# Performance work log

Hardware: AMD Instinct MI355X
Metric: run time of the kernel (lower is better)

Reference implementation:

```python
import jax, jax.numpy as jnp
import numpy as np

EMBED_DIMS = [8, 16, 8]      # prod = 1024 = embed_dim
HIDDEN_DIMS = [16, 16, 16]   # prod = 4096 = hidden_dim
RANK = 16
B, S = 4, 1024


def _make_cores(key, in_dims, out_dims, rank):
    d = len(in_dims)
    ranks = [1] + [rank] * (d - 1) + [1]
    cores = []
    for k in range(d):
        key, sub = jax.random.split(key)
        shape = (ranks[k], in_dims[k], out_dims[k], ranks[k + 1])
        scale = 1.0 / np.sqrt(in_dims[k] * ranks[k])
        cores.append((scale * jax.random.normal(sub, shape, dtype=jnp.float32)))
    return cores


def setup_inputs() -> dict:
    key = jax.random.key(0)
    k_x, k1, k2, kb1, kb2 = jax.random.split(key, 5)
    x = jax.random.normal(k_x, (B, S, 1024), dtype=jnp.float32)
    fc1 = _make_cores(k1, EMBED_DIMS, HIDDEN_DIMS, RANK)
    fc2 = _make_cores(k2, HIDDEN_DIMS, EMBED_DIMS, RANK)
    b1 = 0.01 * jax.random.normal(kb1, (4096,), dtype=jnp.float32)
    b2 = 0.01 * jax.random.normal(kb2, (1024,), dtype=jnp.float32)
    return {
        "x": x,
        "fc1_c0": fc1[0], "fc1_c1": fc1[1], "fc1_c2": fc1[2], "fc1_b": b1,
        "fc2_c0": fc2[0], "fc2_c1": fc2[1], "fc2_c2": fc2[2], "fc2_b": b2,
    }


def tt_linear(x_flat, cores, bias, in_dims):
    """TT-matrix x batch-of-vectors product. x_flat: [N, prod(in_dims)].

    Cores: core_k has shape [r_{k-1}, n_k, m_k, r_k] with r_0 = r_d = 1.
    Invariant: acc is [r_{k-1}, n_k, rest] with rest laid out as
    (n_{k+1}..n_d, N, m_1..m_{k-1}).
    """
    N = x_flat.shape[0]
    acc = x_flat.reshape((N,) + tuple(in_dims))      # [N, n1..nd]
    acc = jnp.moveaxis(acc, 0, -1)                   # [n1..nd, N]
    acc = acc.reshape(in_dims[0], -1)[None]          # [1, n1, rest]
    d = len(cores)
    for k, c in enumerate(cores):
        # contract previous rank + current input mode
        acc = jnp.einsum('pnR,pnmq->Rmq', acc, c)    # [rest, m_k, r_k]
        if k < d - 1:
            n_next = in_dims[k + 1]
            R, m, q = acc.shape
            acc = acc.reshape(n_next, R // n_next, m, q)
            acc = jnp.transpose(acc, (3, 0, 1, 2)).reshape(q, n_next, -1)
    # final acc: [N * m1..m_{d-1}, m_d, 1] -> [N, M]
    return acc.reshape(N, -1) + bias


def reference(x, fc1_c0, fc1_c1, fc1_c2, fc1_b, fc2_c0, fc2_c1, fc2_c2, fc2_b):
    flat = x.reshape(-1, x.shape[-1])                        # [N, embed_dim]
    z1 = tt_linear(flat, [fc1_c0, fc1_c1, fc1_c2], fc1_b, EMBED_DIMS)   # [N, hidden]
    h1 = jax.nn.gelu(z1, approximate=False)                  # exact erf GELU (torch default)
    z2 = tt_linear(h1, [fc2_c0, fc2_c1, fc2_c2], fc2_b, HIDDEN_DIMS)    # [N, embed]
    return z2.reshape(*x.shape[:-1], z2.shape[-1])
```

## Files before the change

kernel.cpp:

```cpp
#include <hip/hip_runtime.h>
#include <stdint.h>

__device__ __forceinline__ float b2f(unsigned short u) {
    union { uint32_t i; float f; } v; v.i = ((uint32_t)u) << 16; return v.f;
}
__device__ __forceinline__ unsigned short f2b(float f) {
    union { float f; uint32_t i; } v; v.f = f;
    uint32_t r = v.i + 0x7fffu + ((v.i >> 16) & 1u);
    return (unsigned short)(r >> 16);
}

typedef __bf16 bf16x8 __attribute__((ext_vector_type(8)));
typedef float  f32x16 __attribute__((ext_vector_type(16)));

template<int N1, int N2, int N3, int M1, int M2, int M3>
__device__ __forceinline__ void build_W_fused(int blk,
                                              const float* __restrict__ c0,
                                              const float* __restrict__ c1,
                                              const float* __restrict__ c2,
                                              unsigned short* __restrict__ W,
                                              float* __restrict__ S) {
    constexpr int K = N1 * N2 * N3;
    const int n2 = blk / M2;
    const int m2 = blk % M2;

    for (int e = threadIdx.x; e < 16 * N3 * M3; e += 256) {
        const int m3 = e % M3;
        const int n3 = (e / M3) % N3;
        const int r1 = e / (M3 * N3);
        const float* c1p = c1 + ((r1 * N2 + n2) * M2 + m2) * 16;
        float s = 0.f;
#pragma unroll
        for (int r2 = 0; r2 < 16; ++r2)
            s += c1p[r2] * c2[(r2 * N3 + n3) * M3 + m3];
        S[e] = s;
    }
    __syncthreads();

    for (int e = threadIdx.x; e < N1 * M1 * M3; e += 256) {
        const int m3 = e % M3;
        const int m1 = (e / M3) % M1;
        const int n1 = e / (M3 * M1);
        const float* c0p = c0 + (n1 * M1 + m1) * 16;
        float acc[N3] = {};
#pragma unroll
        for (int r1 = 0; r1 < 16; ++r1) {
            const float c0v = c0p[r1];
#pragma unroll
            for (int n3 = 0; n3 < N3; ++n3)
                acc[n3] += c0v * S[(r1 * N3 + n3) * M3 + m3];
        }
        unsigned short ob[N3];
#pragma unroll
        for (int n3 = 0; n3 < N3; ++n3) ob[n3] = f2b(acc[n3]);
        unsigned short* dst = W + (size_t)((m1 * M2 + m2) * M3 + m3) * K
                                + (n1 * N2 + n2) * N3;
#pragma unroll
        for (int c = 0; c < N3 / 8; ++c)
            ((int4*)dst)[c] = ((const int4*)ob)[c];
    }
}

__global__ __launch_bounds__(256)
void prep_all(const float* __restrict__ c10, const float* __restrict__ c11,
              const float* __restrict__ c12,
              const float* __restrict__ c20, const float* __restrict__ c21,
              const float* __restrict__ c22,
              const float* __restrict__ x, unsigned short* __restrict__ xb,
              unsigned short* __restrict__ W1, unsigned short* __restrict__ W2) {
    __shared__ float S[16 * 128];
    const int b = blockIdx.x;
    if (b < 256) {
        build_W_fused<8, 16, 8, 16, 16, 16>(b, c10, c11, c12, W1, S);
    } else if (b < 512) {
        build_W_fused<16, 16, 16, 8, 16, 8>(b - 256, c20, c21, c22, W2, S);
    } else {
        const int t = (b - 512) * 256 + threadIdx.x;
        const float4* p = (const float4*)(x + (size_t)t * 8);
        float4 f0 = p[0], f1 = p[1];
        int4 o;
        o.x = (uint32_t)f2b(f0.x) | ((uint32_t)f2b(f0.y) << 16);
        o.y = (uint32_t)f2b(f0.z) | ((uint32_t)f2b(f0.w) << 16);
        o.z = (uint32_t)f2b(f1.x) | ((uint32_t)f2b(f1.y) << 16);
        o.w = (uint32_t)f2b(f1.z) | ((uint32_t)f2b(f1.w) << 16);
        ((int4*)xb)[t] = o;
    }
}

template<int N3, int M3>
__device__ __forceinline__ void build_T_body(int e,
                                             const float* __restrict__ c1,
                                             const float* __restrict__ c2,
                                             float* __restrict__ T) {
    int m3 = e % M3;
    int t  = e / M3;
    int n3 = t % N3;
    int rm = t / N3;
    float s = 0.f;
#pragma unroll
    for (int r2 = 0; r2 < 16; ++r2)
        s += c1[rm * 16 + r2] * c2[(r2 * N3 + n3) * M3 + m3];
    T[e] = s;
}

__global__ __launch_bounds__(256)
void prep_stage1(const float* __restrict__ c11, const float* __restrict__ c12,
                 float* __restrict__ T1,
                 const float* __restrict__ c21, const float* __restrict__ c22,
                 float* __restrict__ T2,
                 const float* __restrict__ x, unsigned short* __restrict__ xb) {
    const int b = blockIdx.x;
    if (b < 2048) {
        build_T_body<8, 16>(b * 256 + threadIdx.x, c11, c12, T1);
    } else if (b < 4096) {
        build_T_body<16, 8>((b - 2048) * 256 + threadIdx.x, c21, c22, T2);
    } else {
        const int t = (b - 4096) * 256 + threadIdx.x;
        const float4* p = (const float4*)(x + (size_t)t * 8);
        float4 f0 = p[0], f1 = p[1];
        int4 o;
        o.x = (uint32_t)f2b(f0.x) | ((uint32_t)f2b(f0.y) << 16);
        o.y = (uint32_t)f2b(f0.z) | ((uint32_t)f2b(f0.w) << 16);
        o.z = (uint32_t)f2b(f1.x) | ((uint32_t)f2b(f1.y) << 16);
        o.w = (uint32_t)f2b(f1.z) | ((uint32_t)f2b(f1.w) << 16);
        ((int4*)xb)[t] = o;
    }
}

template<int N1, int N2, int N3, int M1, int M2, int M3>
__device__ __forceinline__ void build_W_body(int t,
                                             const float* __restrict__ c0,
                                             const float* __restrict__ T,
                                             unsigned short* __restrict__ W) {
    constexpr int K = N1 * N2 * N3;
    int m3 = t % M3;
    int m2 = (t / M3) % M2;
    int n2 = (t / (M3 * M2)) % N2;
    int m1 = (t / (M3 * M2 * N2)) % M1;
    int n1 =  t / (M3 * M2 * N2 * M1);

    float c0r[16];
    const float4* c0p = (const float4*)(c0 + (n1 * M1 + m1) * 16);
#pragma unroll
    for (int i = 0; i < 4; ++i) ((float4*)c0r)[i] = c0p[i];

    float acc[N3] = {};
#pragma unroll
    for (int r1 = 0; r1 < 16; ++r1) {
        const float* Tp = T + (size_t)(((r1 * 16 + n2) * 16 + m2) * N3) * M3 + m3;
#pragma unroll
        for (int n3 = 0; n3 < N3; ++n3)
            acc[n3] += c0r[r1] * Tp[n3 * M3];
    }

    unsigned short ob[N3];
#pragma unroll
    for (int n3 = 0; n3 < N3; ++n3) ob[n3] = f2b(acc[n3]);

    unsigned short* dst = W + (size_t)((m1 * M2 + m2) * M3 + m3) * K
                            + (n1 * N2 + n2) * N3;
#pragma unroll
    for (int c = 0; c < N3 / 8; ++c)
        ((int4*)dst)[c] = ((const int4*)ob)[c];
}

template<int N1, int N2, int N3, int M1, int M2, int M3>
__global__ __launch_bounds__(256)
void build_W(const float* __restrict__ c0, const float* __restrict__ T,
             unsigned short* __restrict__ W) {
    build_W_body<N1, N2, N3, M1, M2, M3>(blockIdx.x * 256 + threadIdx.x, c0, T, W);
}

template<int BM, int BN, int KTOT, int GX, bool DO_GELU>
__global__ __launch_bounds__(512, 2)
void gemm_8p(const unsigned short* __restrict__ A,
             const unsigned short* __restrict__ Bt,
             const float* __restrict__ bias,
             unsigned short* __restrict__ C,
             int Ncols)
{
    constexpr int BK   = 64;
    constexpr int NT   = KTOT / BK;
    constexpr int AE   = BM * BK;
    constexpr int SLOT = (BM + BN) * BK;
    constexpr int ACH  = (AE * 2) / 1024;
    constexpr int CPW  = ((SLOT * 2) / 1024) / 8;

    extern __shared__ unsigned short sh[];

    const int tid   = threadIdx.x;
    const int lane  = tid & 63;
    const int wave  = tid >> 6;
    const int m32   = lane & 31;
    const int kh    = lane >> 5;
    const int waveM = (wave >> 1) * 64;
    const int waveN = (wave & 1) * 64;
    const int srow8 = lane >> 3;
    const int sslot = lane & 7;

    int lin = (int)blockIdx.y * GX + (int)blockIdx.x;
    const int total = GX * (int)gridDim.y;
    lin = (lin & 7) * (total >> 3) + (lin >> 3);
    const int colBase = (lin % GX) * BN;
    const int rowBase = (lin / GX) * BM;

#define P8_STAGE(TS_, KK_, U_)                                                \
    {                                                                         \
        const int c_   = wave * CPW + (U_);                                   \
        const bool b_  = c_ >= ACH;                                           \
        const int r_   = (b_ ? c_ - ACH : c_) * 8 + srow8;                    \
        const int jg_  = sslot ^ (r_ & 7) ^ ((r_ >> 3) & 7);                  \
        const unsigned short* s_ = (b_ ?                                      \
            Bt + (size_t)(colBase + r_) * KTOT :                              \
            A  + (size_t)(rowBase + r_) * KTOT) + (KK_) + jg_ * 8;            \
        unsigned short* d_ = sh + (TS_) + c_ * 512;                           \
        __builtin_amdgcn_global_load_lds(                                     \
            (const __attribute__((address_space(1))) void*)s_,                \
            (__attribute__((address_space(3))) void*)d_, 16, 0, 0);           \
    }

    f32x16 acc[2][2] = {};

#pragma unroll
    for (int u = 0; u < CPW; ++u) P8_STAGE(0, 0, u)
#pragma unroll
    for (int u = 0; u < CPW; ++u) P8_STAGE(SLOT, BK, u)
    asm volatile("s_waitcnt vmcnt(%0)" :: "n"(CPW) : "memory");
    __builtin_amdgcn_s_barrier();

    for (int t = 0; t < NT; ++t) {
        const unsigned short* Ab = sh + (t % 3) * SLOT;
        const unsigned short* Bb = Ab + AE;
        const int ts = ((t + 2) % 3) * SLOT;
        const int kk = (t + 2) * BK;
        const bool doStage = (t + 2 < NT);

#pragma unroll
        for (int ph = 0; ph < 4; ++ph) {
            bf16x8 af[2], bfr[2];
            const int g = ph * 2 + kh;
#pragma unroll
            for (int i = 0; i < 2; ++i) {
                const int r = waveM + i * 32 + m32;
                const int key = (r & 7) ^ ((r >> 3) & 7);
                af[i] = *(const bf16x8*)&Ab[r * BK + ((g ^ key) << 3)];
            }
#pragma unroll
            for (int j = 0; j < 2; ++j) {
                const int r = waveN + j * 32 + m32;
                const int key = (r & 7) ^ ((r >> 3) & 7);
                bfr[j] = *(const bf16x8*)&Bb[r * BK + ((g ^ key) << 3)];
            }
            if (doStage && ph < 3) {
                P8_STAGE(ts, kk, ph * 2)
                P8_STAGE(ts, kk, ph * 2 + 1)
            }
            __builtin_amdgcn_s_barrier();
            __builtin_amdgcn_s_setprio(1);
#pragma unroll
            for (int i = 0; i < 2; ++i)
#pragma unroll
                for (int j = 0; j < 2; ++j)
                    acc[i][j] = __builtin_amdgcn_mfma_f32_32x32x16_bf16(
                        af[i], bfr[j], acc[i][j], 0, 0, 0);
            __builtin_amdgcn_s_setprio(0);
            __builtin_amdgcn_s_barrier();
        }

        if (t + 2 < NT) {
            asm volatile("s_waitcnt vmcnt(%0)" :: "n"(CPW) : "memory");
        } else if (t + 1 < NT) {
            asm volatile("s_waitcnt vmcnt(0)" ::: "memory");
        }
        if (t + 1 < NT) __builtin_amdgcn_s_barrier();
    }
#undef P8_STAGE

#pragma unroll
    for (int i = 0; i < 2; ++i) {
#pragma unroll
        for (int j = 0; j < 2; ++j) {
            const int col = colBase + waveN + j * 32 + m32;
            const float bv = bias[col];
#pragma unroll
            for (int reg = 0; reg < 16; ++reg) {
                const int row = rowBase + waveM + i * 32 +
                                (reg & 3) + 8 * (reg >> 2) + 4 * kh;
                float z = acc[i][j][reg] + bv;
                if (DO_GELU)
                    z = 0.5f * z * (1.f + erff(z * 0.70710678118654752f));
                C[(size_t)row * Ncols + col] = f2b(z);
            }
        }
    }
}

template<int BM, int BN, int KCH, int KSTR, int GX, int GY,
         bool DO_GELU, bool ATOMIC>
__global__ __launch_bounds__(256, 4)
void gemm_sb(const unsigned short* __restrict__ A,
             const unsigned short* __restrict__ Bt,
             const float* __restrict__ bias,
             void* __restrict__ Cv,
             int Ncols)
{
    constexpr int BK  = 64;
    constexpr int NT  = KCH / BK;
    constexpr int ASZ = BM * BK;
    constexpr int ACH = BM / 32;
    constexpr int BCH = BN / 32;
    constexpr int FI  = BM / 64, FJ = BN / 64;

    extern __shared__ unsigned short sh[];

    const int tid   = threadIdx.x;
    const int lane  = tid & 63;
    const int wave  = tid >> 6;
    const int m32   = lane & 31;
    const int khalf = lane >> 5;
    const int waveM = (wave >> 1) * (BM / 2);
    const int waveN = (wave & 1) * (BN / 2);
    const int srow  = tid >> 3;
    const int sslot = tid & 7;

    int lin = ((int)blockIdx.z * GY + (int)blockIdx.y) * GX + (int)blockIdx.x;
    const int total = GX * GY * (int)gridDim.z;
    lin = (lin & 7) * (total >> 3) + (lin >> 3);
    const int colBase = (lin % GX) * BN;
    const int rowBase = ((lin / GX) % GY) * BM;
    const int kOff    = (lin / (GX * GY)) * KCH;

#define SB_STAGE(K0_)                                                         \
    {                                                                         \
        _Pragma("unroll")                                                     \
        for (int c = 0; c < ACH; ++c) {                                       \
            const int r  = c * 32 + srow;                                     \
            const int jg = sslot ^ (r & 7) ^ ((r >> 3) & 7);                  \
            const unsigned short* src = A +                                   \
                (size_t)(rowBase + r) * KSTR + (K0_) + jg * 8;                \
            unsigned short* dst = sh + c * 2048 + wave * 512;                 \
            __builtin_amdgcn_global_load_lds(                                 \
                (const __attribute__((address_space(1))) void*)src,           \
                (__attribute__((address_space(3))) void*)dst, 16, 0, 0);      \
        }                                                                     \
        _Pragma("unroll")                                                     \
        for (int c = 0; c < BCH; ++c) {                                       \
            const int r  = c * 32 + srow;                                     \
            const int jg = sslot ^ (r & 7) ^ ((r >> 3) & 7);                  \
            const unsigned short* src = Bt +                                  \
                (size_t)(colBase + r) * KSTR + (K0_) + jg * 8;                \
            unsigned short* dst = sh + ASZ + c * 2048 + wave * 512;           \
            __builtin_amdgcn_global_load_lds(                                 \
                (const __attribute__((address_space(1))) void*)src,           \
                (__attribute__((address_space(3))) void*)dst, 16, 0, 0);      \
        }                                                                     \
    }

    f32x16 acc[FI][FJ] = {};

    for (int t = 0; t < NT; ++t) {
        SB_STAGE(kOff + t * BK)
        __syncthreads();

        const unsigned short* Ab = sh;
        const unsigned short* Bb = sh + ASZ;
#pragma unroll
        for (int ks = 0; ks < 4; ++ks) {
            bf16x8 a_f[FI], b_f[FJ];
            const int g = ks * 2 + khalf;
#pragma unroll
            for (int i = 0; i < FI; ++i) {
                const int r = waveM + i * 32 + m32;
                const int key = (r & 7) ^ ((r >> 3) & 7);
                a_f[i] = *(const bf16x8*)&Ab[r * BK + ((g ^ key) << 3)];
            }
#pragma unroll
            for (int j = 0; j < FJ; ++j) {
                const int r = waveN + j * 32 + m32;
                const int key = (r & 7) ^ ((r >> 3) & 7);
                b_f[j] = *(const bf16x8*)&Bb[r * BK + ((g ^ key) << 3)];
            }
#pragma unroll
            for (int i = 0; i < FI; ++i)
#pragma unroll
                for (int j = 0; j < FJ; ++j)
                    acc[i][j] = __builtin_amdgcn_mfma_f32_32x32x16_bf16(
                        a_f[i], b_f[j], acc[i][j], 0, 0, 0);
        }
        if (t + 1 < NT) __syncthreads();
    }
#undef SB_STAGE

#pragma unroll
    for (int i = 0; i < FI; ++i) {
#pragma unroll
        for (int j = 0; j < FJ; ++j) {
            const int col = colBase + waveN + j * 32 + m32;
            const float bv = ATOMIC ? 0.f : bias[col];
#pragma unroll
            for (int reg = 0; reg < 16; ++reg) {
                const int row = rowBase + waveM + i * 32 +
                                (reg & 3) + 8 * (reg >> 2) + 4 * khalf;
                const size_t off = (size_t)row * Ncols + col;
                if (ATOMIC) {
                    unsafeAtomicAdd((float*)Cv + off, acc[i][j][reg]);
                } else {
                    float z = acc[i][j][reg] + bv;
                    if (DO_GELU) {
                        z = 0.5f * z * (1.f + erff(z * 0.70710678118654752f));
                        ((unsigned short*)Cv)[off] = f2b(z);
                    } else {
                        ((float*)Cv)[off] = z;
                    }
                }
            }
        }
    }
}

#define PC_COMPUTE(BUF)                                                       \
    {                                                                         \
        _Pragma("unroll")                                                     \
        for (int ks = 0; ks < 4; ++ks) {                                      \
            bf16x8 a_f[FI], b_f[FJ];                                          \
            _Pragma("unroll")                                                 \
            for (int i = 0; i < FI; ++i) {                                    \
                const int key = (m32 & 7) ^                                   \
                    (((waveM >> 3) + 4 * i + (m32 >> 3)) & 7);                \
                const int slot = ((ks * 2 + khalf) ^ key) * 8;                \
                a_f[i] = *(const bf16x8*)&As[(BUF) * ASZ +                    \
                          (waveM + i * 32 + m32) * BK + slot];                \
            }                                                                 \
            _Pragma("unroll")                                                 \
            for (int j = 0; j < FJ; ++j) {                                    \
                const int key = (m32 & 7) ^                                   \
                    (((waveN >> 3) + 4 * j + (m32 >> 3)) & 7);                \
                const int slot = ((ks * 2 + khalf) ^ key) * 8;                \
                b_f[j] = *(const bf16x8*)&Bs[(BUF) * BSZ +                    \
                          (waveN + j * 32 + m32) * BK + slot];                \
            }                                                                 \
            _Pragma("unroll")                                                 \
            for (int i = 0; i < FI; ++i)                                      \
                _Pragma("unroll")                                             \
                for (int j = 0; j < FJ; ++j)                                  \
                    acc[i][j] = __builtin_amdgcn_mfma_f32_32x32x16_bf16(      \
                        a_f[i], b_f[j], acc[i][j], 0, 0, 0);                  \
        }                                                                     \
    }

template<int BM, int BN, int KTOT, bool DO_GELU, bool A_F32, bool C_F32>
__global__ __launch_bounds__(512, 4)
void gemm_pc(const void* __restrict__ Av,
             const unsigned short* __restrict__ Bt,
             const float* __restrict__ bias,
             void* __restrict__ Cv,
             int Ncols) {
    constexpr int BK  = 64;
    constexpr int CA  = BM / 8;
    constexpr int CB  = BN / 8;
    constexpr int PA  = CA / 4;
    constexpr int PB  = CB / 4;
    constexpr int FI  = BM / 64;
    constexpr int FJ  = BN / 64;
    constexpr int ASZ = BM * BK;
    constexpr int BSZ = BN * BK;
    __shared__ unsigned short As[2 * ASZ];
    __shared__ unsigned short Bs[2 * BSZ];

    const int tid  = threadIdx.x;
    const int lane = tid & 63;
    const int wave = tid >> 6;
    const int rowBase = blockIdx.y * BM;
    const int colBase = blockIdx.x * BN;

    const int lr    = lane >> 3;
    const int jj    = lane & 7;
    const int m32   = lane & 31;
    const int khalf = lane >> 5;

    if (wave >= 4) {
        const int pw = wave - 4;
#pragma unroll
        for (int it = 0; it < PA; ++it) {
            const int c  = pw * PA + it;
            const int jg = jj ^ lr ^ (c & 7);
            const size_t aoff = (size_t)(rowBase + c * 8 + lr) * KTOT + jg * 8;
            int4 v;
            if (A_F32) {
                const float* ga = (const float*)Av + aoff;
                float4 f0 = *(const float4*)ga;
                float4 f1 = *(const float4*)(ga + 4);
                v.x = (uint32_t)f2b(f0.x) | ((uint32_t)f2b(f0.y) << 16);
                v.y = (uint32_t)f2b(f0.z) | ((uint32_t)f2b(f0.w) << 16);
                v.z = (uint32_t)f2b(f1.x) | ((uint32_t)f2b(f1.y) << 16);
                v.w = (uint32_t)f2b(f1.z) | ((uint32_t)f2b(f1.w) << 16);
            } else {
                v = *(const int4*)((const unsigned short*)Av + aoff);
            }
            *(int4*)&As[c * 512 + lane * 8] = v;
        }
#pragma unroll
        for (int it = 0; it < PB; ++it) {
            const int c  = pw * PB + it;
            const int jg = jj ^ lr ^ (c & 7);
            *(int4*)&Bs[c * 512 + lane * 8] =
                *(const int4*)(Bt + (size_t)(colBase + c * 8 + lr) * KTOT + jg * 8);
        }
        __syncthreads();

        int buf = 1;
        for (int k0 = BK; k0 < KTOT; k0 += BK) {
            int4 aR[PA], bR[PB];
#pragma unroll
            for (int it = 0; it < PA; ++it) {
                const int c  = pw * PA + it;
                const int jg = jj ^ lr ^ (c & 7);
                const size_t aoff = (size_t)(rowBase + c * 8 + lr) * KTOT + k0 + jg * 8;
                if (A_F32) {
                    const float* ga = (const float*)Av + aoff;
                    float4 f0 = *(const float4*)ga;
                    float4 f1 = *(const float4*)(ga + 4);
                    int4 v;
                    v.x = (uint32_t)f2b(f0.x) | ((uint32_t)f2b(f0.y) << 16);
                    v.y = (uint32_t)f2b(f0.z) | ((uint32_t)f2b(f0.w) << 16);
                    v.z = (uint32_t)f2b(f1.x) | ((uint32_t)f2b(f1.y) << 16);
                    v.w = (uint32_t)f2b(f1.z) | ((uint32_t)f2b(f1.w) << 16);
                    aR[it] = v;
                } else {
                    aR[it] = *(const int4*)((const unsigned short*)Av + aoff);
                }
            }
#pragma unroll
            for (int it = 0; it < PB; ++it) {
                const int c  = pw * PB + it;
                const int jg = jj ^ lr ^ (c & 7);
                bR[it] = *(const int4*)(Bt + (size_t)(colBase + c * 8 + lr) * KTOT + k0 + jg * 8);
            }
#pragma unroll
            for (int it = 0; it < PA; ++it) {
                const int c = pw * PA + it;
                *(int4*)&As[buf * ASZ + c * 512 + lane * 8] = aR[it];
            }
#pragma unroll
            for (int it = 0; it < PB; ++it) {
                const int c = pw * PB + it;
                *(int4*)&Bs[buf * BSZ + c * 512 + lane * 8] = bR[it];
            }
            __syncthreads();
            buf ^= 1;
        }
    } else {
        const int waveM = (wave >> 1) * (BM / 2);
        const int waveN = (wave & 1) * (BN / 2);
        f32x16 acc[FI][FJ] = {};

        __syncthreads();

        int cur = 0;
        for (int k0 = BK; k0 < KTOT; k0 += BK) {
            PC_COMPUTE(cur)
            __syncthreads();
            cur ^= 1;
        }
        PC_COMPUTE(cur)

#pragma unroll
        for (int i = 0; i < FI; ++i) {
#pragma unroll
            for (int j = 0; j < FJ; ++j) {
                const int col = colBase + waveN + j * 32 + m32;
                const float bv = bias[col];
#pragma unroll
                for (int reg = 0; reg < 16; ++reg) {
                    const int row = rowBase + waveM + i * 32 +
                                    (reg & 3) + 8 * (reg >> 2) + 4 * khalf;
                    float z = acc[i][j][reg] + bv;
                    if (DO_GELU)
                        z = 0.5f * z * (1.f + erff(z * 0.70710678118654752f));
                    const size_t off = (size_t)row * Ncols + col;
                    if (C_F32) ((float*)Cv)[off] = z;
                    else       ((unsigned short*)Cv)[off] = f2b(z);
                }
            }
        }
    }
}

extern "C" void kernel_launch(void* const* d_in, const int* in_sizes, int n_in,
                              void* d_out, int out_size, void* d_ws, size_t ws_size,
                              hipStream_t stream) {
    const float* x      = (const float*)d_in[0];
    const float* fc1_c0 = (const float*)d_in[1];
    const float* fc1_c1 = (const float*)d_in[2];
    const float* fc1_c2 = (const float*)d_in[3];
    const float* fc1_b  = (const float*)d_in[4];
    const float* fc2_c0 = (const float*)d_in[5];
    const float* fc2_c1 = (const float*)d_in[6];
    const float* fc2_c2 = (const float*)d_in[7];
    const float* fc2_b  = (const float*)d_in[8];

    char* ws = (char*)d_ws;
    const bool big = ws_size >= (48ull << 20);

    constexpr int DLDS8 = 3 * (256 + 128) * 64 * 2;
    constexpr int DLDS  = 40 << 10;

    static bool attr_done = false;
    if (!attr_done) {
        attr_done = true;
        (void)hipFuncSetAttribute(
            reinterpret_cast<const void*>(&gemm_8p<256, 128, 1024, 32, true>),
            hipFuncAttributeMaxDynamicSharedMemorySize, DLDS8);
    }

    if (big) {
        unsigned short* xb = (unsigned short*)d_out;
        unsigned short* W1 = (unsigned short*)ws;
        unsigned short* W2 = (unsigned short*)(ws + (8u << 20));
        unsigned short* h  = (unsigned short*)(ws + (16u << 20));

        prep_all<<<2560, 256, 0, stream>>>(fc1_c0, fc1_c1, fc1_c2,
                                           fc2_c0, fc2_c1, fc2_c2,
                                           x, xb, W1, W2);
        gemm_8p<256, 128, 1024, 32, true>
            <<<dim3(32, 16), 512, DLDS8, stream>>>(xb, W1, fc1_b, h, 4096);
        gemm_sb<128, 64, 4096, 4096, 16, 32, false, false>
            <<<dim3(16, 32, 1), 256, DLDS, stream>>>(h, W2, fc2_b, d_out, 1024);
    } else {
        float* T1 = (float*)d_out;
        float* T2 = (float*)d_out + 524288;
        unsigned short* xb = (unsigned short*)((char*)d_out + (4u << 20));
        unsigned short* W = (unsigned short*)ws;
        unsigned short* h = (unsigned short*)(ws + (8u << 20));

        prep_stage1<<<6144, 256, 0, stream>>>(fc1_c1, fc1_c2, T1,
                                              fc2_c1, fc2_c2, T2, x, xb);
        build_W<8, 16, 8, 16, 16, 16><<<2048, 256, 0, stream>>>(fc1_c0, T1, W);
        gemm_pc<128, 128, 1024, true, false, false>
            <<<dim3(32, 32), 512, 0, stream>>>(xb, W, fc1_b, h, 4096);
        build_W<16, 16, 16, 8, 16, 8><<<1024, 256, 0, stream>>>(fc2_c0, T2, W);
        gemm_pc<128, 64, 4096, false, false, true>
            <<<dim3(16, 32), 512, 0, stream>>>(h, W, fc2_b, d_out, 1024);
    }
}
```

Baseline: 211.0 us.

## Replace fc1 GEMM with 256x256 tile, double-buffered kernel using 128x64 wave tiles

The first GEMM moves from a 256x128 block tile with a three-stage, phase-interleaved LDS pipeline to a 256x256 tile where each wave computes a 128x64 sub-tile (4x2 MFMA fragments). Staging becomes a simple double buffer: the next K slice is issued, then a full __syncthreads per iteration. The intent is to raise arithmetic intensity per LDS and global byte and halve the number of blocks. The trade-offs are that the finer barrier and priority interleaving are dropped, and only 256 blocks are launched, which may underfill the GPU's compute units.

```diff
diff --git a/kernel.cpp b/kernel.cpp
--- a/kernel.cpp
+++ b/kernel.cpp
@@ -173,18 +173,19 @@
 
 template<int BM, int BN, int KTOT, int GX, bool DO_GELU>
 __global__ __launch_bounds__(512, 2)
-void gemm_8p(const unsigned short* __restrict__ A,
-             const unsigned short* __restrict__ Bt,
-             const float* __restrict__ bias,
-             unsigned short* __restrict__ C,
-             int Ncols)
+void gemm_big(const unsigned short* __restrict__ A,
+              const unsigned short* __restrict__ Bt,
+              const float* __restrict__ bias,
+              unsigned short* __restrict__ C,
+              int Ncols)
 {
     constexpr int BK   = 64;
     constexpr int NT   = KTOT / BK;
-    constexpr int AE   = BM * BK;
-    constexpr int SLOT = (BM + BN) * BK;
-    constexpr int ACH  = (AE * 2) / 1024;
-    constexpr int CPW  = ((SLOT * 2) / 1024) / 8;
+    constexpr int ASZ  = BM * BK;
+    constexpr int BUFE = (BM + BN) * BK;
+    constexpr int ACH  = BM / 64;
+    constexpr int BCH  = BN / 64;
+    constexpr int FI   = 4, FJ = 2;
 
     extern __shared__ unsigned short sh[];
 
@@ -192,11 +193,11 @@
     const int lane  = tid & 63;
     const int wave  = tid >> 6;
     const int m32   = lane & 31;
-    const int kh    = lane >> 5;
-    const int waveM = (wave >> 1) * 64;
-    const int waveN = (wave & 1) * 64;
-    const int srow8 = lane >> 3;
-    const int sslot = lane & 7;
+    const int khalf = lane >> 5;
+    const int waveM = (wave >> 2) * 128;
+    const int waveN = (wave & 3) * 64;
+    const int srow  = tid >> 3;
+    const int sslot = tid & 7;
 
     int lin = (int)blockIdx.y * GX + (int)blockIdx.x;
     const int total = GX * (int)gridDim.y;
@@ -204,88 +205,82 @@
     const int colBase = (lin % GX) * BN;
     const int rowBase = (lin / GX) * BM;
 
-#define P8_STAGE(TS_, KK_, U_)                                                \
+#define BG_STAGE(B_, K0_)                                                     \
     {                                                                         \
-        const int c_   = wave * CPW + (U_);                                   \
-        const bool b_  = c_ >= ACH;                                           \
-        const int r_   = (b_ ? c_ - ACH : c_) * 8 + srow8;                    \
-        const int jg_  = sslot ^ (r_ & 7) ^ ((r_ >> 3) & 7);                  \
-        const unsigned short* s_ = (b_ ?                                      \
-            Bt + (size_t)(colBase + r_) * KTOT :                              \
-            A  + (size_t)(rowBase + r_) * KTOT) + (KK_) + jg_ * 8;            \
-        unsigned short* d_ = sh + (TS_) + c_ * 512;                           \
-        __builtin_amdgcn_global_load_lds(                                     \
-            (const __attribute__((address_space(1))) void*)s_,                \
-            (__attribute__((address_space(3))) void*)d_, 16, 0, 0);           \
-    }
-
-    f32x16 acc[2][2] = {};
-
-#pragma unroll
-    for (int u = 0; u < CPW; ++u) P8_STAGE(0, 0, u)
-#pragma unroll
-    for (int u = 0; u < CPW; ++u) P8_STAGE(SLOT, BK, u)
-    asm volatile("s_waitcnt vmcnt(%0)" :: "n"(CPW) : "memory");
-    __builtin_amdgcn_s_barrier();
-
+        _Pragma("unroll")                                                     \
+        for (int c = 0; c < ACH; ++c) {                                       \
+            const int r  = c * 64 + srow;                                     \
+            const int jg = sslot ^ (r & 7) ^ ((r >> 3) & 7);                  \
+            const unsigned short* src = A +                                   \
+                (size_t)(rowBase + r) * KTOT + (K0_) + jg * 8;                \
+            unsigned short* dst = sh + (B_) * BUFE + c * 4096 + wave * 512;   \
+            __builtin_amdgcn_global_load_lds(                                 \
+                (const __attribute__((address_space(1))) void*)src,           \
+                (__attribute__((address_space(3))) void*)dst, 16, 0, 0);      \
+        }                                                                     \
+        _Pragma("unroll")                                                     \
+        for (int c = 0; c < BCH; ++c) {                                       \
+            const int r  = c * 64 + srow;                                     \
+            const int jg = sslot ^ (r & 7) ^ ((r >> 3) & 7);                  \
+            const unsigned short* src = Bt +                                  \
+                (size_t)(colBase + r) * KTOT + (K0_) + jg * 8;                \
+            unsigned short* dst = sh + (B_) * BUFE + ASZ + c * 4096           \
+                                  + wave * 512;                               \
+            __builtin_amdgcn_global_load_lds(                                 \
+                (const __attribute__((address_space(1))) void*)src,           \
+                (__attribute__((address_space(3))) void*)dst, 16, 0, 0);      \
+        }                                                                     \
+    }
+
+    f32x16 acc[FI][FJ] = {};
+
+    BG_STAGE(0, 0)
+    __syncthreads();
+
+    int buf = 0;
     for (int t = 0; t < NT; ++t) {
-        const unsigned short* Ab = sh + (t % 3) * SLOT;
-        const unsigned short* Bb = Ab + AE;
-        const int ts = ((t + 2) % 3) * SLOT;
-        const int kk = (t + 2) * BK;
-        const bool doStage = (t + 2 < NT);
-
-#pragma unroll
-        for (int ph = 0; ph < 4; ++ph) {
-            bf16x8 af[2], bfr[2];
-            const int g = ph * 2 + kh;
-#pragma unroll
-            for (int i = 0; i < 2; ++i) {
+        if (t + 1 < NT) BG_STAGE(buf ^ 1, (t + 1) * BK)
+
+        const unsigned short* Ab = sh + buf * BUFE;
+        const unsigned short* Bb = Ab + ASZ;
+#pragma unroll
+        for (int ks = 0; ks < 4; ++ks) {
+            bf16x8 a_f[FI], b_f[FJ];
+            const int g = ks * 2 + khalf;
+#pragma unroll
+            for (int i = 0; i < FI; ++i) {
                 const int r = waveM + i * 32 + m32;
                 const int key = (r & 7) ^ ((r >> 3) & 7);
-                af[i] = *(const bf16x8*)&Ab[r * BK + ((g ^ key) << 3)];
-            }
-#pragma unroll
-            for (int j = 0; j < 2; ++j) {
+                a_f[i] = *(const bf16x8*)&Ab[r * BK + ((g ^ key) << 3)];
+            }
+#pragma unroll
+            for (int j = 0; j < FJ; ++j) {
                 const int r = waveN + j * 32 + m32;
                 const int key = (r & 7) ^ ((r >> 3) & 7);
-                bfr[j] = *(const bf16x8*)&Bb[r * BK + ((g ^ key) << 3)];
-            }
-            if (doStage && ph < 3) {
-                P8_STAGE(ts, kk, ph * 2)
-                P8_STAGE(ts, kk, ph * 2 + 1)
-            }
-            __builtin_amdgcn_s_barrier();
-            __builtin_amdgcn_s_setprio(1);
-#pragma unroll
-            for (int i = 0; i < 2; ++i)
-#pragma unroll
-                for (int j = 0; j < 2; ++j)
+                b_f[j] = *(const bf16x8*)&Bb[r * BK + ((g ^ key) << 3)];
+            }
+#pragma unroll
+            for (int i = 0; i < FI; ++i)
+#pragma unroll
+                for (int j = 0; j < FJ; ++j)
                     acc[i][j] = __builtin_amdgcn_mfma_f32_32x32x16_bf16(
-                        af[i], bfr[j], acc[i][j], 0, 0, 0);
-            __builtin_amdgcn_s_setprio(0);
-            __builtin_amdgcn_s_barrier();
-        }
-
-        if (t + 2 < NT) {
-            asm volatile("s_waitcnt vmcnt(%0)" :: "n"(CPW) : "memory");
-        } else if (t + 1 < NT) {
-            asm volatile("s_waitcnt vmcnt(0)" ::: "memory");
-        }
-        if (t + 1 < NT) __builtin_amdgcn_s_barrier();
-    }
-#undef P8_STAGE
-
-#pragma unroll
-    for (int i = 0; i < 2; ++i) {
-#pragma unroll
-        for (int j = 0; j < 2; ++j) {
+                        a_f[i], b_f[j], acc[i][j], 0, 0, 0);
+        }
+        __syncthreads();
+        buf ^= 1;
+    }
+#undef BG_STAGE
+
+#pragma unroll
+    for (int i = 0; i < FI; ++i) {
+#pragma unroll
+        for (int j = 0; j < FJ; ++j) {
             const int col = colBase + waveN + j * 32 + m32;
             const float bv = bias[col];
 #pragma unroll
             for (int reg = 0; reg < 16; ++reg) {
                 const int row = rowBase + waveM + i * 32 +
-                                (reg & 3) + 8 * (reg >> 2) + 4 * kh;
+                                (reg & 3) + 8 * (reg >> 2) + 4 * khalf;
                 float z = acc[i][j][reg] + bv;
                 if (DO_GELU)
                     z = 0.5f * z * (1.f + erff(z * 0.70710678118654752f));
@@ -602,15 +597,15 @@
     char* ws = (char*)d_ws;
     const bool big = ws_size >= (48ull << 20);
 
-    constexpr int DLDS8 = 3 * (256 + 128) * 64 * 2;
+    constexpr int DLDSB = 2 * (256 + 256) * 64 * 2;
     constexpr int DLDS  = 40 << 10;
 
     static bool attr_done = false;
     if (!attr_done) {
         attr_done = true;
         (void)hipFuncSetAttribute(
-            reinterpret_cast<const void*>(&gemm_8p<256, 128, 1024, 32, true>),
-            hipFuncAttributeMaxDynamicSharedMemorySize, DLDS8);
+            reinterpret_cast<const void*>(&gemm_big<256, 256, 1024, 16, true>),
+            hipFuncAttributeMaxDynamicSharedMemorySize, DLDSB);
     }
 
     if (big) {
@@ -622,8 +617,8 @@
         prep_all<<<2560, 256, 0, stream>>>(fc1_c0, fc1_c1, fc1_c2,
                                            fc2_c0, fc2_c1, fc2_c2,
                                            x, xb, W1, W2);
-        gemm_8p<256, 128, 1024, 32, true>
-            <<<dim3(32, 16), 512, DLDS8, stream>>>(xb, W1, fc1_b, h, 4096);
+        gemm_big<256, 256, 1024, 16, true>
+            <<<dim3(16, 16), 512, DLDSB, stream>>>(xb, W1, fc1_b, h, 4096);
         gemm_sb<128, 64, 4096, 4096, 16, 32, false, false>
             <<<dim3(16, 32, 1), 256, DLDS, stream>>>(h, W2, fc2_b, d_out, 1024);
     } else {
```

Measured after the change: 201.3 us, median of 2. 1.05x faster.
